# Performance work log

Measured on AMD Instinct MI355X. Metric: run time of the kernel, lower is better.

The kernel has to match this reference:

```python
import jax, jax.numpy as jnp
from jax import lax
import numpy as np
import math

B_SZ, SEQ, D_MODEL = 2, 2048, 2048
D_INNER, D_STATE, D_CONV, HEADS, P, CHUNK = 4096, 128, 4, 64, 64, 128
CONV_DIM = D_INNER + 2 * D_STATE
D_IN_PROJ = 2 * D_INNER + 2 * D_STATE + HEADS


def setup_inputs() -> dict:
    key = jax.random.key(0)
    ks = jax.random.split(key, 6)
    hidden_states = jax.random.normal(ks[0], (B_SZ, SEQ, D_MODEL), jnp.float32)
    W_in = jax.random.normal(ks[1], (D_IN_PROJ, D_MODEL), jnp.float32) * 0.02
    W_conv = jax.random.normal(ks[2], (CONV_DIM, 1, D_CONV), jnp.float32) * 0.2
    b_conv = jnp.zeros((CONV_DIM,), jnp.float32)
    A_log = jnp.log(jnp.arange(1, HEADS + 1, dtype=jnp.float32))
    D = jnp.ones((HEADS,), jnp.float32)
    # dt_bias init as in the torch module
    dt = jnp.exp(jax.random.uniform(ks[3], (HEADS,)) * (math.log(0.1) - math.log(0.001)) + math.log(0.001))
    dt = jnp.clip(dt, 1e-4, None)
    dt_bias = dt + jnp.log(-jnp.expm1(-dt))
    norm_weight = jnp.ones((D_INNER,), jnp.float32)
    W_out = jax.random.normal(ks[4], (D_MODEL, D_INNER), jnp.float32) * 0.02
    return {"hidden_states": hidden_states, "W_in": W_in, "W_conv": W_conv, "b_conv": b_conv,
            "A_log": A_log, "D": D, "dt_bias": dt_bias, "norm_weight": norm_weight, "W_out": W_out}


def _mamba2_core(hidden_states, W_in, W_conv, b_conv, A_log, D, dt_bias, norm_weight, W_out):
    Bsz, L, _ = hidden_states.shape
    NC = L // CHUNK
    zxbcdt = hidden_states @ W_in.T                         # [B,L,d_in_proj]
    z = zxbcdt[..., :D_INNER]
    xBC = zxbcdt[..., D_INNER:D_INNER + CONV_DIM]
    dt = zxbcdt[..., -HEADS:]
    # causal depthwise conv1d over sequence
    xc = jnp.swapaxes(xBC, 1, 2)                            # [B,C,L]
    xc = lax.conv_general_dilated(xc, W_conv, (1,), [(D_CONV - 1, 0)],
                                  feature_group_count=CONV_DIM,
                                  dimension_numbers=('NCH', 'OIH', 'NCH'))
    xc = xc + b_conv[None, :, None]
    xBC = jax.nn.silu(jnp.swapaxes(xc, 1, 2))               # [B,L,conv_dim]
    x = xBC[..., :D_INNER]
    Bm = xBC[..., D_INNER:D_INNER + D_STATE]                # num_groups=1
    Cm = xBC[..., -D_STATE:]
    dt = jax.nn.softplus(dt + dt_bias)                      # [B,L,H]; dt_limit (0,inf) is a no-op
    A = -jnp.exp(A_log)                                     # [H]
    # --- chunked SSD scan (chunk_size = CHUNK), same math as torch_ssm ---
    xch = x.reshape(Bsz, NC, CHUNK, HEADS, P)
    dtc = dt.reshape(Bsz, NC, CHUNK, HEADS)
    Bc = Bm.reshape(Bsz, NC, CHUNK, D_STATE)
    Cc = Cm.reshape(Bsz, NC, CHUNK, D_STATE)
    u = xch * dtc[..., None]                                # [b,c,l,h,p]
    dA = dtc * A                                            # [b,c,l,h]
    dA_cs = jnp.cumsum(dA, axis=2)                          # [b,c,l,h]
    # within-chunk causal attention-like term
    seg = dA_cs[:, :, :, None, :] - dA_cs[:, :, None, :, :] # [b,c,l,s,h]
    mask = jnp.tril(jnp.ones((CHUNK, CHUNK), bool))
    Lmat = jnp.exp(jnp.where(mask[None, None, :, :, None], seg, -jnp.inf))
    CB = jnp.einsum('bcln,bcsn->bcls', Cc, Bc)
    M = CB[..., None] * Lmat                                # [b,c,l,s,h]
    Y_diag = jnp.einsum('bclsh,bcshp->bclhp', M, u)
    # per-chunk final states
    decay_states = jnp.exp(dA_cs[:, :, -1:, :] - dA_cs)     # [b,c,l,h]
    states = jnp.einsum('bcln,bclh,bclhp->bchpn', Bc, decay_states, u)
    chunk_decay = jnp.exp(dA_cs[:, :, -1, :])               # [b,c,h]
    # inter-chunk recurrence over NC chunks
    def step(h, inp):
        st, cd = inp                                        # [b,h,p,n], [b,h]
        h_new = h * cd[:, :, None, None] + st
        return h_new, h                                     # emit state at chunk start
    sts = jnp.moveaxis(states, 1, 0)
    cds = jnp.moveaxis(chunk_decay, 1, 0)
    h0 = jnp.zeros((Bsz, HEADS, P, D_STATE), hidden_states.dtype)
    _, h_starts = lax.scan(step, h0, (sts, cds))
    h_starts = jnp.moveaxis(h_starts, 0, 1)                 # [b,c,h,p,n]
    state_decay_out = jnp.exp(dA_cs)                        # [b,c,l,h]
    Y_off = jnp.einsum('bcln,bclh,bchpn->bclhp', Cc, state_decay_out, h_starts)
    Y = Y_diag + Y_off + D[None, None, None, :, None] * xch
    y = Y.reshape(Bsz, L, D_INNER)
    # gated RMSNorm (gate first, then norm; group_size == d_inner)
    yg = y * jax.nn.silu(z)
    var = jnp.mean(yg * yg, axis=-1, keepdims=True)
    y = yg * lax.rsqrt(var + 1e-5) * norm_weight
    return y @ W_out.T


def reference(hidden_states, W_in, W_conv, b_conv, A_log, D, dt_bias, norm_weight, W_out):
    return _mamba2_core(hidden_states, W_in, W_conv, b_conv, A_log, D, dt_bias, norm_weight, W_out)
```

## Files before the change

kernel.cpp:

```cpp
#include <hip/hip_runtime.h>
#include <hip/hip_bf16.h>
#include <stdint.h>

typedef __bf16 bf16;
typedef __bf16 bf16x8 __attribute__((ext_vector_type(8)));
typedef __bf16 bf16x4 __attribute__((ext_vector_type(4)));
typedef float f32x4v __attribute__((ext_vector_type(4)));

#define SEQ    2048
#define DMODEL 2048
#define DI     4096
#define NH     64
#define PDIM   64
#define CHUNKL 128
#define NCH    16
#define CONVD  4352
#define DPROJ  8512
#define ZLD    8704
#define NTOK   4096
#define LP     136

__device__ __forceinline__ float sigmoid_f(float x){ return 1.f/(1.f+expf(-x)); }
__device__ __forceinline__ float silu_f(float x){ return x*sigmoid_f(x); }
__device__ __forceinline__ float softplus_f(float x){ return x > 20.f ? x : log1pf(expf(x)); }

__global__ __launch_bounds__(256) void cvt_all_kernel(const float* __restrict__ hs,
                                                      const float* __restrict__ W_in,
                                                      const float* __restrict__ W_out,
                                                      bf16* __restrict__ hsb,
                                                      bf16* __restrict__ winb,
                                                      bf16* __restrict__ woutb){
    int blk = blockIdx.x;
    if (blk < 8192){
        int i = (blk*256 + threadIdx.x)*4;
        float4 v = *(const float4*)&hs[i];
        bf16x4 o; o[0]=(bf16)v.x; o[1]=(bf16)v.y; o[2]=(bf16)v.z; o[3]=(bf16)v.w;
        *(bf16x4*)&hsb[i] = o;
    } else if (blk < 25600){
        int i = ((blk-8192)*256 + threadIdx.x)*4;
        int r = i >> 11;
        bf16x4 o;
        if (r < DPROJ){
            float4 v = *(const float4*)&W_in[i];
            o[0]=(bf16)v.x; o[1]=(bf16)v.y; o[2]=(bf16)v.z; o[3]=(bf16)v.w;
        } else {
            o[0]=(bf16)0.f; o[1]=(bf16)0.f; o[2]=(bf16)0.f; o[3]=(bf16)0.f;
        }
        *(bf16x4*)&winb[i] = o;
    } else {
        int i = ((blk-25600)*256 + threadIdx.x)*4;
        float4 v = *(const float4*)&W_out[i];
        bf16x4 o; o[0]=(bf16)v.x; o[1]=(bf16)v.y; o[2]=(bf16)v.z; o[3]=(bf16)v.w;
        *(bf16x4*)&woutb[i] = o;
    }
}

#define READ_A(BUFP, QM)                                                               \
    {                                                                                  \
        _Pragma("unroll")                                                              \
        for (int i=0;i<4;i++)                                                          \
            _Pragma("unroll")                                                          \
            for (int k2=0;k2<2;k2++)                                                   \
                af[i][k2] = *(const bf16x8*)&(BUFP)[aoff[i][k2] + (QM)*8192];          \
    }

#define READ_B(BUFP, QN, BFR)                                                          \
    {                                                                                  \
        _Pragma("unroll")                                                              \
        for (int nf=0;nf<2;nf++)                                                       \
            _Pragma("unroll")                                                          \
            for (int k2=0;k2<2;k2++)                                                   \
                BFR[nf][k2] = *(const bf16x8*)&(BUFP)[boff[nf][k2] + (QN)*8192];       \
    }

#define MMA_Q(QM, QN, BFR)                                                             \
    {                                                                                  \
        __builtin_amdgcn_s_setprio(1);                                                 \
        _Pragma("unroll")                                                              \
        for (int i=0;i<4;i++)                                                          \
            _Pragma("unroll")                                                          \
            for (int nf=0;nf<2;nf++)                                                   \
                _Pragma("unroll")                                                      \
                for (int k2=0;k2<2;k2++)                                               \
                    acc[(QM)*4+i][(QN)*2+nf] = __builtin_amdgcn_mfma_f32_16x16x32_bf16( \
                        af[i][k2], BFR[nf][k2], acc[(QM)*4+i][(QN)*2+nf], 0,0,0);      \
        __builtin_amdgcn_s_setprio(0);                                                 \
    }

#define SBAR() do { __builtin_amdgcn_sched_barrier(0);                                 \
                    __builtin_amdgcn_s_barrier();                                      \
                    asm volatile("s_waitcnt lgkmcnt(0)" ::: "memory");                 \
                    __builtin_amdgcn_sched_barrier(0); } while(0)

__global__ __launch_bounds__(512) void gemm1_kernel(const bf16* __restrict__ A,
                                                    const bf16* __restrict__ Bmat,
                                                    bf16* __restrict__ Cz,
                                                    float* __restrict__ tpart,
                                                    int NXB, int NYB, int K){
    __shared__ __align__(16) bf16 lds[2][2*16384];
    const int tid  = threadIdx.x;
    const int w    = tid >> 6;
    const int lane = tid & 63;
    const int wm   = w >> 2, wn = w & 3;
    const int bid  = blockIdx.x;

    int aoff[4][2], boff[2][2];
    #pragma unroll
    for (int i=0;i<4;i++)
        #pragma unroll
        for (int k2=0;k2<2;k2++){
            int ra0 = wm*64 + i*16 + (lane&15);
            int slot = (k2*4 + (lane>>4)) ^ (ra0&7);
            aoff[i][k2] = ra0*64 + slot*8;
        }
    #pragma unroll
    for (int nf=0;nf<2;nf++)
        #pragma unroll
        for (int k2=0;k2<2;k2++){
            int rb0 = wn*32 + nf*16 + (lane&15);
            int slot = (k2*4 + (lane>>4)) ^ (rb0&7);
            boff[nf][k2] = 16384 + rb0*64 + slot*8;
        }
    const int er = (lane>>4)*4, ec = lane&15;

    if (bid < 256){
        int kz  = bid >> 6;
        int t64 = bid & 63;
        const int tn2 = 8192 + (t64 & 3)*128;
        const int tm2 = (t64 >> 2)*256;
        const int kt0 = kz*8;

        const bf16* srcA2[2][2];
        const bf16* srcB2[2];
        #pragma unroll
        for (int r0h=0;r0h<2;r0h++)
            #pragma unroll
            for (int i=0;i<2;i++){
                int lr = r0h*128 + i*64 + (tid>>3);
                int growA = tm2 + ((lr>>6)&1)*128 + (lr>>7)*64 + (lr&63);
                int gslot = (tid&7) ^ (lr&7);
                srcA2[r0h][i] = A + (long)growA*K + gslot*8;
            }
        #pragma unroll
        for (int i=0;i<2;i++){
            int lr = i*64 + (tid>>3);
            int gslot = (tid&7) ^ (lr&7);
            srcB2[i] = Bmat + (long)(tn2 + lr)*K + gslot*8;
        }
        auto stA = [&](int buf, int t, int r0h){
            long koff = (long)(kt0 + t)*64;
            #pragma unroll
            for (int i=0;i<2;i++){
                bf16* dst = &lds[buf][0] + (size_t)(r0h*128 + i*64 + w*8)*64;
                __builtin_amdgcn_global_load_lds(
                    (const __attribute__((address_space(1))) void*)(srcA2[r0h][i] + koff),
                    (__attribute__((address_space(3))) void*)dst, 16, 0, 0);
            }
        };
        auto stB = [&](int buf, int t){
            long koff = (long)(kt0 + t)*64;
            #pragma unroll
            for (int i=0;i<2;i++){
                bf16* dst = &lds[buf][16384] + (size_t)(i*64 + w*8)*64;
                __builtin_amdgcn_global_load_lds(
                    (const __attribute__((address_space(1))) void*)(srcB2[i] + koff),
                    (__attribute__((address_space(3))) void*)dst, 16, 0, 0);
            }
        };

        f32x4v acc2[8][2];
        #pragma unroll
        for (int i=0;i<8;i++)
            #pragma unroll
            for (int j=0;j<2;j++) acc2[i][j] = {0.f,0.f,0.f,0.f};
        bf16x8 af[4][2], bfr0[2][2];

        stA(0,0,0); stA(0,0,1); stB(0,0);
        __syncthreads();
        int cur = 0;
        for (int t=0; t<8; ++t){
            int nxt = cur ^ 1;
            const bf16* bufc = &lds[cur][0];
            if (t+1 < 8){ stA(nxt,t+1,0); stA(nxt,t+1,1); stB(nxt,t+1); }
            READ_A(bufc, 0)
            READ_B(bufc, 0, bfr0)
            #pragma unroll
            for (int i=0;i<4;i++)
                #pragma unroll
                for (int nf=0;nf<2;nf++)
                    #pragma unroll
                    for (int k2=0;k2<2;k2++)
                        acc2[i][nf] = __builtin_amdgcn_mfma_f32_16x16x32_bf16(
                            af[i][k2], bfr0[nf][k2], acc2[i][nf], 0,0,0);
            READ_A(bufc, 1)
            #pragma unroll
            for (int i=0;i<4;i++)
                #pragma unroll
                for (int nf=0;nf<2;nf++)
                    #pragma unroll
                    for (int k2=0;k2<2;k2++)
                        acc2[4+i][nf] = __builtin_amdgcn_mfma_f32_16x16x32_bf16(
                            af[i][k2], bfr0[nf][k2], acc2[4+i][nf], 0,0,0);
            __syncthreads();
            cur = nxt;
        }
        #pragma unroll
        for (int mi=0;mi<8;mi++)
            #pragma unroll
            for (int nf=0;nf<2;nf++){
                long r0 = tm2 + wm*128 + mi*16 + er;
                int  c0 = tn2 + wn*32 + nf*16 + ec;
                #pragma unroll
                for (int j=0;j<4;j++)
                    tpart[((long)kz*4096 + (r0+j))*512 + (c0 - 8192)] = acc2[mi][nf][j];
            }
        return;
    }

    int bid2 = bid - 256;
    int wg   = (bid2 & 7)*64 + (bid2 >> 3);
    const int SW = 8;
    int sup = wg / (SW*NYB);
    int rr  = wg % (SW*NYB);
    int x0  = sup*SW;
    int wl  = (NXB - x0 < SW) ? (NXB - x0) : SW;
    int x   = x0 + rr % wl;
    int y   = rr / wl;
    const int tm = y*256, tn = x*256;
    const int KT = K >> 6;

    f32x4v acc[8][4];
    #pragma unroll
    for (int i=0;i<8;i++)
        #pragma unroll
        for (int j=0;j<4;j++) acc[i][j] = {0.f,0.f,0.f,0.f};
    bf16x8 af[4][2];
    bf16x8 bfr0[2][2], bfr1[2][2];

    const bf16* srcA[2][2];
    const bf16* srcB[2][2];
    #pragma unroll
    for (int r0h=0;r0h<2;r0h++)
        #pragma unroll
        for (int i=0;i<2;i++){
            int lr = r0h*128 + i*64 + (tid>>3);
            int growA = tm + ((lr>>6)&1)*128 + (lr>>7)*64 + (lr&63);
            int growB = tn + ((lr>>5)&3)*64 + (lr>>7)*32 + (lr&31);
            int gslot = (tid&7) ^ (lr&7);
            srcA[r0h][i] = A + (long)growA*K + gslot*8;
            srcB[r0h][i] = Bmat + (long)growB*K + gslot*8;
        }

    auto stageA = [&](int buf, int t, int r0h){
        long koff = (long)t*64;
        #pragma unroll
        for (int i=0;i<2;i++){
            bf16* dst = &lds[buf][0] + (size_t)(r0h*128 + i*64 + w*8)*64;
            __builtin_amdgcn_global_load_lds(
                (const __attribute__((address_space(1))) void*)(srcA[r0h][i] + koff),
                (__attribute__((address_space(3))) void*)dst, 16, 0, 0);
        }
    };
    auto stageB = [&](int buf, int t, int r0h){
        long koff = (long)t*64;
        #pragma unroll
        for (int i=0;i<2;i++){
            bf16* dst = &lds[buf][16384] + (size_t)(r0h*128 + i*64 + w*8)*64;
            __builtin_amdgcn_global_load_lds(
                (const __attribute__((address_space(1))) void*)(srcB[r0h][i] + koff),
                (__attribute__((address_space(3))) void*)dst, 16, 0, 0);
        }
    };

    stageA(0, 0, 0); stageB(0, 0, 0); stageA(0, 0, 1); stageB(0, 0, 1);
    if (KT > 1){ stageA(1, 1, 0); stageB(1, 1, 0); stageA(1, 1, 1); stageB(1, 1, 1); }
    asm volatile("s_waitcnt vmcnt(8)" ::: "memory");
    __builtin_amdgcn_s_barrier();

    int cur = 0;
    for (int t = 0; t < KT; ++t){
        int nxt = cur ^ 1;
        const bf16* bufc = &lds[cur][0];
        READ_A(bufc, 0)
        READ_B(bufc, 0, bfr0)
        READ_B(bufc, 1, bfr1)
        if (t+1 < KT){ asm volatile("s_waitcnt vmcnt(8)" ::: "memory"); }
        else         { asm volatile("s_waitcnt vmcnt(0)" ::: "memory"); }
        SBAR();
        MMA_Q(0, 0, bfr0)
        MMA_Q(0, 1, bfr1)
        __builtin_amdgcn_sched_barrier(0);
        if (t+2 < KT){ stageA(cur, t+2, 0); stageB(cur, t+2, 0); }
        READ_A(bufc, 1)
        SBAR();
        MMA_Q(1, 0, bfr0)
        MMA_Q(1, 1, bfr1)
        __builtin_amdgcn_sched_barrier(0);
        if (t+2 < KT){ stageA(cur, t+2, 1); stageB(cur, t+2, 1); }
        cur = nxt;
    }

    #pragma unroll
    for (int mi=0;mi<8;mi++)
        #pragma unroll
        for (int ni=0;ni<4;ni++){
            long r0 = tm + wm*128 + mi*16 + er;
            int  c0 = tn + wn*64 + ni*16 + ec;
            #pragma unroll
            for (int j=0;j<4;j++)
                Cz[(r0+j)*ZLD + c0] = (bf16)acc[mi][ni][j];
        }
}

__global__ __launch_bounds__(512) void gemm256x128_kernel(const bf16* __restrict__ A,
                                                          const bf16* __restrict__ Bmat,
                                                          float* __restrict__ C,
                                                          int NXB, int NYB, int K, int ldc){
    __shared__ __align__(16) bf16 lds[3][24576];
    const int tid  = threadIdx.x;
    const int w    = tid >> 6;
    const int lane = tid & 63;
    const int wm   = w >> 2, wn = w & 3;

    int bid = blockIdx.x, nb = gridDim.x;
    int wg = (bid & 7)*(nb >> 3) + (bid >> 3);
    const int SW = 8;
    int sup = wg / (SW*NYB);
    int rr  = wg % (SW*NYB);
    int x0  = sup*SW;
    int wl  = (NXB - x0 < SW) ? (NXB - x0) : SW;
    int x   = x0 + rr % wl;
    int y   = rr / wl;
    const int tm = y*256, tn = x*128;
    const int KT = K >> 6;

    f32x4v acc[8][2];
    #pragma unroll
    for (int i=0;i<8;i++)
        #pragma unroll
        for (int j=0;j<2;j++) acc[i][j] = {0.f,0.f,0.f,0.f};
    bf16x8 af[4][2];
    bf16x8 bfr[2][2];

    const bf16* srcA[2][2];
    const bf16* srcB[2];
    #pragma unroll
    for (int r0h=0;r0h<2;r0h++)
        #pragma unroll
        for (int i=0;i<2;i++){
            int lr = r0h*128 + i*64 + (tid>>3);
            int growA = tm + ((lr>>6)&1)*128 + (lr>>7)*64 + (lr&63);
            int gslot = (tid&7) ^ (lr&7);
            srcA[r0h][i] = A + (long)growA*K + gslot*8;
        }
    #pragma unroll
    for (int i=0;i<2;i++){
        int lr = i*64 + (tid>>3);
        int gslot = (tid&7) ^ (lr&7);
        srcB[i] = Bmat + (long)(tn + lr)*K + gslot*8;
    }
    int aoff[4][2], boff[2][2];
    #pragma unroll
    for (int i=0;i<4;i++)
        #pragma unroll
        for (int k2=0;k2<2;k2++){
            int ra0 = wm*64 + i*16 + (lane&15);
            int slot = (k2*4 + (lane>>4)) ^ (ra0&7);
            aoff[i][k2] = ra0*64 + slot*8;
        }
    #pragma unroll
    for (int nf=0;nf<2;nf++)
        #pragma unroll
        for (int k2=0;k2<2;k2++){
            int rb0 = wn*32 + nf*16 + (lane&15);
            int slot = (k2*4 + (lane>>4)) ^ (rb0&7);
            boff[nf][k2] = 16384 + rb0*64 + slot*8;
        }

    auto stageA = [&](int buf, int t, int r0h){
        long koff = (long)t*64;
        #pragma unroll
        for (int i=0;i<2;i++){
            bf16* dst = &lds[buf][0] + (size_t)(r0h*128 + i*64 + w*8)*64;
            __builtin_amdgcn_global_load_lds(
                (const __attribute__((address_space(1))) void*)(srcA[r0h][i] + koff),
                (__attribute__((address_space(3))) void*)dst, 16, 0, 0);
        }
    };
    auto stageB = [&](int buf, int t){
        long koff = (long)t*64;
        #pragma unroll
        for (int i=0;i<2;i++){
            bf16* dst = &lds[buf][16384] + (size_t)(i*64 + w*8)*64;
            __builtin_amdgcn_global_load_lds(
                (const __attribute__((address_space(1))) void*)(srcB[i] + koff),
                (__attribute__((address_space(3))) void*)dst, 16, 0, 0);
        }
    };

    stageA(0, 0, 0); stageA(0, 0, 1); stageB(0, 0);
    if (KT > 1){ stageA(1, 1, 0); stageA(1, 1, 1); stageB(1, 1); }
    asm volatile("s_waitcnt vmcnt(6)" ::: "memory");
    __builtin_amdgcn_s_barrier();

    int cur = 0;
    for (int t = 0; t < KT; ++t){
        int stb = cur + 2; if (stb >= 3) stb -= 3;
        const bf16* bufc = &lds[cur][0];
        READ_A(bufc, 0)
        READ_B(bufc, 0, bfr)
        if (t+2 < KT){ stageA(stb, t+2, 0); stageA(stb, t+2, 1); }
        SBAR();
        MMA_Q(0, 0, bfr)
        READ_A(bufc, 1)
        if (t+2 < KT){
            stageB(stb, t+2);
            asm volatile("s_waitcnt vmcnt(6)" ::: "memory");
        } else {
            asm volatile("s_waitcnt vmcnt(0)" ::: "memory");
        }
        SBAR();
        MMA_Q(1, 0, bfr)
        cur = (cur == 2) ? 0 : cur + 1;
    }

    const int er = (lane>>4)*4, ec = lane&15;
    #pragma unroll
    for (int mi=0;mi<8;mi++)
        #pragma unroll
        for (int ni=0;ni<2;ni++){
            long r0 = tm + wm*128 + mi*16 + er;
            int  c0 = tn + wn*32 + ni*16 + ec;
            #pragma unroll
            for (int j=0;j<4;j++)
                C[(r0+j)*ldc + c0] = acc[mi][ni][j];
        }
}

__global__ __launch_bounds__(256) void tailreduce_kernel(const float* __restrict__ p,
                                                         bf16* __restrict__ zx,
                                                         float* __restrict__ dtf){
    long i = ((long)blockIdx.x*256 + threadIdx.x)*4;
    int r = (int)(i >> 9);
    int c = (int)(i & 511);
    const long Q = (long)4096*512;
    float4 a  = *(const float4*)&p[i];
    float4 b  = *(const float4*)&p[i+Q];
    float4 cc = *(const float4*)&p[i+2*Q];
    float4 d  = *(const float4*)&p[i+3*Q];
    float s0 = a.x+b.x+cc.x+d.x, s1 = a.y+b.y+cc.y+d.y;
    float s2 = a.z+b.z+cc.z+d.z, s3 = a.w+b.w+cc.w+d.w;
    bf16x4 o; o[0]=(bf16)s0; o[1]=(bf16)s1; o[2]=(bf16)s2; o[3]=(bf16)s3;
    *(bf16x4*)&zx[(long)r*ZLD + 8192 + c] = o;
    int col = 8192 + c;
    float sv[4] = {s0,s1,s2,s3};
    #pragma unroll
    for (int j=0;j<4;j++){
        int cj = col + j;
        if (cj >= 8448 && cj < 8512) dtf[(long)r*64 + (cj-8448)] = sv[j];
    }
}

__global__ __launch_bounds__(256) void mid1_kernel(const bf16* __restrict__ zx,
                                                   const float* __restrict__ Wc,
                                                   const float* __restrict__ bc,
                                                   const float* __restrict__ dtf,
                                                   const float* __restrict__ A_log,
                                                   const float* __restrict__ dt_bias,
                                                   bf16* __restrict__ xc,
                                                   float* __restrict__ dtv,
                                                   float* __restrict__ dacs,
                                                   float* __restrict__ cdec){
    int blk = blockIdx.x;
    if (blk < 2560){
        int by = blk/5, bx = blk%5;
        int c4 = bx*256 + threadIdx.x;
        if (c4 >= 1088) return;
        int ch = c4*4;
        int b = by >> 8, t0 = (by & 255)*8;
        float4 tap[4];
        #pragma unroll
        for (int e=0;e<4;e++) tap[e] = *(const float4*)&Wc[(ch+e)*4];
        float4 bq = *(const float4*)&bc[ch];
        float bca[4] = {bq.x, bq.y, bq.z, bq.w};
        const bf16* col = zx + (long)(b*SEQ)*ZLD + 4096 + ch;
        bf16x4 v[11];
        #pragma unroll
        for (int k=0;k<11;k++){
            int t = t0 - 3 + k;
            if (t >= 0) v[k] = *(const bf16x4*)&col[(long)t*ZLD];
            else { v[k][0]=(bf16)0.f; v[k][1]=(bf16)0.f; v[k][2]=(bf16)0.f; v[k][3]=(bf16)0.f; }
        }
        #pragma unroll
        for (int j=0;j<8;j++){
            bf16x4 o;
            #pragma unroll
            for (int e=0;e<4;e++){
                float acc = bca[e] + (float)v[j][e]*tap[e].x + (float)v[j+1][e]*tap[e].y
                                   + (float)v[j+2][e]*tap[e].z + (float)v[j+3][e]*tap[e].w;
                o[e] = (bf16)silu_f(acc);
            }
            *(bf16x4*)&xc[(long)(b*SEQ + t0 + j)*CONVD + ch] = o;
        }
    } else {
        int wid  = ((blk-2560)*256 + threadIdx.x) >> 6;
        int lane = threadIdx.x & 63;
        int h  = wid & 63, bc2 = wid >> 6;
        int b  = bc2 >> 4,  c  = bc2 & 15;
        float Ah   = -expf(A_log[h]);
        float bias = dt_bias[h];
        long tok0 = (long)(b*SEQ + c*CHUNKL);
        int l0 = lane*2;
        float d0 = softplus_f(dtf[(tok0+l0)*64 + h] + bias);
        float d1 = softplus_f(dtf[(tok0+l0+1)*64 + h] + bias);
        float s = (d0 + d1)*Ah;
        #pragma unroll
        for (int off=1; off<64; off<<=1){
            float t = __shfl_up(s, off, 64);
            if (lane >= off) s += t;
        }
        long base_h = (long)wid*128;
        float cs1 = s;
        float cs0 = s - d1*Ah;
        dtv[base_h+l0]   = d0;  dtv[base_h+l0+1]  = d1;
        dacs[base_h+l0]  = cs0; dacs[base_h+l0+1] = cs1;
        if (lane == 63) cdec[wid] = expf(cs1);
    }
}

__global__ __launch_bounds__(256) void cb_mfma_kernel(const bf16* __restrict__ xc,
                                                      float* __restrict__ cb,
                                                      bf16* __restrict__ BT){
    __shared__ __align__(16) bf16 A1[128*LP];
    __shared__ __align__(16) bf16 B1[128*LP];
    int blk = blockIdx.x;  int b = blk>>4, c = blk&15;
    int tid = threadIdx.x;
    const int w = tid >> 6, lane = tid & 63;
    long tok0 = (long)(b*SEQ + c*CHUNKL);
    int l = tid>>1, n0 = (tid&1)*64;
    const bf16* crow = xc + tok0*CONVD + (long)l*CONVD;
    #pragma unroll
    for (int v=0;v<8;v++){
        *(bf16x8*)&A1[l*LP + n0 + v*8] = *(const bf16x8*)&crow[4224 + n0 + v*8];
        *(bf16x8*)&B1[l*LP + n0 + v*8] = *(const bf16x8*)&crow[4096 + n0 + v*8];
    }
    __syncthreads();
    f32x4v acc[2][8];
    #pragma unroll
    for (int mi=0;mi<2;mi++)
        #pragma unroll
        for (int ni=0;ni<8;ni++) acc[mi][ni] = {0.f,0.f,0.f,0.f};
    #pragma unroll
    for (int kk=0; kk<128; kk+=32){
        bf16x8 afr[2], bfr2[8];
        #pragma unroll
        for (int mi=0;mi<2;mi++)
            afr[mi] = *(const bf16x8*)&A1[(w*32 + mi*16 + (lane&15))*LP + kk + (lane>>4)*8];
        #pragma unroll
        for (int ni=0;ni<8;ni++)
            bfr2[ni] = *(const bf16x8*)&B1[(ni*16 + (lane&15))*LP + kk + (lane>>4)*8];
        #pragma unroll
        for (int mi=0;mi<2;mi++)
            #pragma unroll
            for (int ni=0;ni<8;ni++)
                acc[mi][ni] = __builtin_amdgcn_mfma_f32_16x16x32_bf16(afr[mi], bfr2[ni], acc[mi][ni], 0,0,0);
    }
    float* out = cb + (long)blk*16384;
    #pragma unroll
    for (int mi=0;mi<2;mi++)
        #pragma unroll
        for (int ni=0;ni<8;ni++){
            int r0 = w*32 + mi*16 + (lane>>4)*4;
            int c0 = ni*16 + (lane&15);
            #pragma unroll
            for (int j=0;j<4;j++) out[(long)(r0+j)*128 + c0] = acc[mi][ni][j];
        }
    {
        int n = tid>>1, s0 = (tid&1)*64;
        bf16* btp = BT + (long)blk*16384 + (long)n*128 + s0;
        #pragma unroll
        for (int v=0;v<8;v++){
            bf16x8 o;
            #pragma unroll
            for (int e=0;e<8;e++) o[e] = B1[(s0+v*8+e)*LP + n];
            *(bf16x8*)&btp[v*8] = o;
        }
    }
}

__global__ __launch_bounds__(256) void states_mfma_kernel(const bf16* __restrict__ xc,
                                                          const bf16* __restrict__ BT,
                                                          const float* __restrict__ dtv,
                                                          const float* __restrict__ dacs,
                                                          bf16* __restrict__ states){
    __shared__ __align__(16) bf16 A1[64*LP];
    __shared__ __align__(16) bf16 B1[128*LP];
    __shared__ float wgtl[128];
    int blk = blockIdx.x;
    int h = blk & 63, bc = blk >> 6;
    int b = bc >> 4, c = bc & 15;
    int tid = threadIdx.x;
    const int w = tid >> 6, lane = tid & 63;
    long tok0 = (long)(b*SEQ + c*CHUNKL);
    long base_h = (long)blk*128;
    float cs_last = dacs[base_h + 127];
    if (tid < 128) wgtl[tid] = dtv[base_h+tid] * expf(cs_last - dacs[base_h+tid]);
    __syncthreads();
    #pragma unroll
    for (int t=0;t<4;t++){
        int l = (tid>>3) + t*32;
        int p0 = (tid&7)*8;
        bf16x8 xv = *(const bf16x8*)&xc[(tok0+l)*CONVD + h*64 + p0];
        float wv = wgtl[l];
        #pragma unroll
        for (int e=0;e<8;e++) A1[(p0+e)*LP + l] = (bf16)((float)xv[e]*wv);
    }
    {
        int n = tid>>1, l0 = (tid&1)*64;
        const bf16* btp = BT + (long)bc*16384 + (long)n*128 + l0;
        #pragma unroll
        for (int v=0;v<8;v++)
            *(bf16x8*)&B1[n*LP + l0 + v*8] = *(const bf16x8*)&btp[v*8];
    }
    __syncthreads();
    f32x4v acc[8];
    #pragma unroll
    for (int ni=0;ni<8;ni++) acc[ni] = {0.f,0.f,0.f,0.f};
    #pragma unroll
    for (int kk=0; kk<128; kk+=32){
        bf16x8 afr = *(const bf16x8*)&A1[(w*16 + (lane&15))*LP + kk + (lane>>4)*8];
        #pragma unroll
        for (int ni=0;ni<8;ni++){
            bf16x8 bfr2 = *(const bf16x8*)&B1[(ni*16 + (lane&15))*LP + kk + (lane>>4)*8];
            acc[ni] = __builtin_amdgcn_mfma_f32_16x16x32_bf16(afr, bfr2, acc[ni], 0,0,0);
        }
    }
    bf16* out = states + (long)blk*8192;
    #pragma unroll
    for (int ni=0;ni<8;ni++){
        int p0 = w*16 + (lane>>4)*4;
        int n  = ni*16 + (lane&15);
        #pragma unroll
        for (int j=0;j<4;j++) out[(long)(p0+j)*128 + n] = (bf16)acc[ni][j];
    }
}

__global__ __launch_bounds__(256) void scan_kernel(const bf16* __restrict__ states,
                                                   const float* __restrict__ cdec,
                                                   bf16* __restrict__ hst){
    long gid = (long)blockIdx.x*256 + threadIdx.x;
    int n = gid & 127;
    int p = (gid >> 7) & 63;
    int h = (gid >> 13) & 63;
    int b = (int)(gid >> 19);
    float hrun = 0.f;
    for (int c=0;c<16;c++){
        long idx = ((((long)(b*16 + c)*64 + h)*64 + p)*128) + n;
        hst[idx] = (bf16)hrun;
        hrun = hrun * cdec[(b*16+c)*64 + h] + (float)states[idx];
    }
}

__global__ __launch_bounds__(256) void yfused_kernel(const bf16* __restrict__ xc,
                                                     const float* __restrict__ cb,
                                                     const bf16* __restrict__ hst,
                                                     const float* __restrict__ dtv,
                                                     const float* __restrict__ dacs,
                                                     bf16* __restrict__ Ybf){
    __shared__ __align__(16) bf16 A1[128*LP];
    __shared__ __align__(16) bf16 B1[64*LP];
    __shared__ float csl[128];
    int blk = blockIdx.x;
    int h = blk & 63, bc = blk >> 6;
    int b = bc >> 4, c = bc & 15;
    int tid = threadIdx.x;
    const int w = tid >> 6, lane = tid & 63;
    long tok0 = (long)(b*SEQ + c*CHUNKL);
    long base_h = (long)blk*128;
    if (tid < 128) csl[tid] = dacs[base_h + tid];
    __syncthreads();
    {
        int l = tid>>1, s0 = (tid&1)*64;
        float el = csl[l];
        const float* cbrow = cb + (long)bc*16384 + (long)l*128 + s0;
        int jend = l - s0; if (jend > 63) jend = 63;
        for (int j=0; j<=jend; j++)
            A1[l*LP + s0 + j] = (bf16)(cbrow[j]*expf(el - csl[s0+j]));
        for (int j=jend+1; j<64; j++)
            A1[l*LP + s0 + j] = (bf16)0.f;
    }
    #pragma unroll
    for (int t=0;t<4;t++){
        int s = (tid>>3) + t*32;
        int p0 = (tid&7)*8;
        bf16x8 xv = *(const bf16x8*)&xc[(tok0+s)*CONVD + h*64 + p0];
        float wv = dtv[base_h + s];
        #pragma unroll
        for (int e=0;e<8;e++) B1[(p0+e)*LP + s] = (bf16)((float)xv[e]*wv);
    }
    __syncthreads();
    f32x4v acc[2][4];
    #pragma unroll
    for (int mi=0;mi<2;mi++)
        #pragma unroll
        for (int ni=0;ni<4;ni++) acc[mi][ni] = {0.f,0.f,0.f,0.f};
    #pragma unroll
    for (int kk=0; kk<128; kk+=32){
        bf16x8 afr[2], bfr2[4];
        #pragma unroll
        for (int mi=0;mi<2;mi++)
            afr[mi] = *(const bf16x8*)&A1[(w*32 + mi*16 + (lane&15))*LP + kk + (lane>>4)*8];
        #pragma unroll
        for (int ni=0;ni<4;ni++)
            bfr2[ni] = *(const bf16x8*)&B1[(ni*16 + (lane&15))*LP + kk + (lane>>4)*8];
        #pragma unroll
        for (int mi=0;mi<2;mi++)
            #pragma unroll
            for (int ni=0;ni<4;ni++)
                acc[mi][ni] = __builtin_amdgcn_mfma_f32_16x16x32_bf16(afr[mi], bfr2[ni], acc[mi][ni], 0,0,0);
    }
    __syncthreads();
    {
        int l = tid>>1, n0 = (tid&1)*64;
        float e1 = expf(csl[l]);
        const bf16* crow = xc + (tok0+l)*CONVD + 4224;
        #pragma unroll
        for (int v=0;v<8;v++){
            bf16x8 cv = *(const bf16x8*)&crow[n0 + v*8];
            bf16x8 o;
            #pragma unroll
            for (int e=0;e<8;e++) o[e] = (bf16)((float)cv[e]*e1);
            *(bf16x8*)&A1[l*LP + n0 + v*8] = o;
        }
    }
    {
        int p = tid>>2, n0 = (tid&3)*32;
        const bf16* hrow = hst + (long)blk*8192 + (long)p*128 + n0;
        #pragma unroll
        for (int v=0;v<4;v++)
            *(bf16x8*)&B1[p*LP + n0 + v*8] = *(const bf16x8*)&hrow[v*8];
    }
    __syncthreads();
    #pragma unroll
    for (int kk=0; kk<128; kk+=32){
        bf16x8 afr[2], bfr2[4];
        #pragma unroll
        for (int mi=0;mi<2;mi++)
            afr[mi] = *(const bf16x8*)&A1[(w*32 + mi*16 + (lane&15))*LP + kk + (lane>>4)*8];
        #pragma unroll
        for (int ni=0;ni<4;ni++)
            bfr2[ni] = *(const bf16x8*)&B1[(ni*16 + (lane&15))*LP + kk + (lane>>4)*8];
        #pragma unroll
        for (int mi=0;mi<2;mi++)
            #pragma unroll
            for (int ni=0;ni<4;ni++)
                acc[mi][ni] = __builtin_amdgcn_mfma_f32_16x16x32_bf16(afr[mi], bfr2[ni], acc[mi][ni], 0,0,0);
    }
    #pragma unroll
    for (int mi=0;mi<2;mi++)
        #pragma unroll
        for (int ni=0;ni<4;ni++){
            int l0 = w*32 + mi*16 + (lane>>4)*4;
            int p  = ni*16 + (lane&15);
            #pragma unroll
            for (int j=0;j<4;j++)
                Ybf[(tok0 + l0 + j)*DI + h*64 + p] = (bf16)acc[mi][ni][j];
        }
}

__global__ __launch_bounds__(256) void gatenorm_kernel(const bf16* __restrict__ Ybf,
                                                       const bf16* __restrict__ zx,
                                                       const bf16* __restrict__ xc,
                                                       const float* __restrict__ Dp,
                                                       const float* __restrict__ nw,
                                                       bf16* __restrict__ ybn){
    __shared__ float red[4];
    int tok = blockIdx.x, tid = threadIdx.x;
    const bf16* yrow = Ybf + (long)tok*DI;
    const bf16* zrow = zx  + (long)tok*ZLD;
    const bf16* xrow = xc  + (long)tok*CONVD;
    float yg[16];
    float ss = 0.f;
    #pragma unroll
    for (int k=0;k<2;k++){
        int d = (tid + k*256)*8;
        bf16x8 yv = *(const bf16x8*)&yrow[d];
        bf16x8 zv = *(const bf16x8*)&zrow[d];
        bf16x8 xv = *(const bf16x8*)&xrow[d];
        float dh = Dp[d>>6];
        #pragma unroll
        for (int e=0;e<8;e++){
            float yy = (float)yv[e] + dh*(float)xv[e];
            float g = yy*silu_f((float)zv[e]);
            yg[k*8+e] = g;
            ss += g*g;
        }
    }
    #pragma unroll
    for (int off=32; off>0; off>>=1) ss += __shfl_down(ss, off, 64);
    if ((tid & 63) == 0) red[tid>>6] = ss;
    __syncthreads();
    float tot = red[0]+red[1]+red[2]+red[3];
    float scale = rsqrtf(tot/(float)DI + 1e-5f);
    #pragma unroll
    for (int k=0;k<2;k++){
        int d = (tid + k*256)*8;
        float4 w0 = *(const float4*)&nw[d];
        float4 w1 = *(const float4*)&nw[d+4];
        float wv[8] = {w0.x,w0.y,w0.z,w0.w,w1.x,w1.y,w1.z,w1.w};
        bf16x8 o;
        #pragma unroll
        for (int e=0;e<8;e++) o[e] = (bf16)(yg[k*8+e]*scale*wv[e]);
        *(bf16x8*)&ybn[(long)tok*DI + d] = o;
    }
}

extern "C" void kernel_launch(void* const* d_in, const int* in_sizes, int n_in,
                              void* d_out, int out_size, void* d_ws, size_t ws_size,
                              hipStream_t stream){
    const float* hs      = (const float*)d_in[0];
    const float* W_in    = (const float*)d_in[1];
    const float* W_conv  = (const float*)d_in[2];
    const float* b_conv  = (const float*)d_in[3];
    const float* A_log   = (const float*)d_in[4];
    const float* Dp      = (const float*)d_in[5];
    const float* dt_bias = (const float*)d_in[6];
    const float* nw      = (const float*)d_in[7];
    const float* W_out   = (const float*)d_in[8];
    float* out = (float*)d_out;

    char* ws = (char*)d_ws;
    const size_t OFF_ZX    = 0;
    const size_t OFF_DTF   = 71303168;
    const size_t OFF_XC    = 72351744;
    const size_t OFF_DTV   = 108003328;
    const size_t OFF_DACS  = 109051904;
    const size_t OFF_CDEC  = 110100480;
    const size_t OFF_CB    = 110108672;
    const size_t OFF_SLOTA = 112205824;
    const size_t OFF_SLOTB = 179314688;
    const size_t OFF_WOUTB = 212869120;

    bf16*  zx    = (bf16*)(ws + OFF_ZX);
    float* dtf   = (float*)(ws + OFF_DTF);
    bf16*  xc    = (bf16*)(ws + OFF_XC);
    float* dtv   = (float*)(ws + OFF_DTV);
    float* dacs  = (float*)(ws + OFF_DACS);
    float* cdec  = (float*)(ws + OFF_CDEC);
    float* cbuf  = (float*)(ws + OFF_CB);
    bf16*  hsb   = (bf16*)(ws + OFF_SLOTA);
    bf16*  winb  = (bf16*)(ws + OFF_SLOTA + 16777216);
    bf16*  states= (bf16*)(ws + OFF_SLOTA);
    bf16*  Ybf   = (bf16*)(ws + OFF_SLOTA);
    float* tpart = (float*)(ws + OFF_SLOTB);
    bf16*  BTb   = (bf16*)(ws + OFF_SLOTB);
    bf16*  hst   = (bf16*)(ws + OFF_SLOTB);
    bf16*  ybn   = (bf16*)(ws + OFF_SLOTB);
    bf16*  woutb = (bf16*)(ws + OFF_WOUTB);

    cvt_all_kernel<<<33792, 256, 0, stream>>>(hs, W_in, W_out, hsb, winb, woutb);

    gemm1_kernel<<<768, 512, 0, stream>>>(hsb, winb, zx, tpart, 32, 16, DMODEL);
    tailreduce_kernel<<<2048, 256, 0, stream>>>(tpart, zx, dtf);

    mid1_kernel<<<3072, 256, 0, stream>>>(zx, W_conv, b_conv, dtf, A_log, dt_bias,
                                          xc, dtv, dacs, cdec);
    cb_mfma_kernel<<<32, 256, 0, stream>>>(xc, cbuf, BTb);
    states_mfma_kernel<<<2048, 256, 0, stream>>>(xc, BTb, dtv, dacs, states);
    scan_kernel<<<4096, 256, 0, stream>>>(states, cdec, hst);
    yfused_kernel<<<2048, 256, 0, stream>>>(xc, cbuf, hst, dtv, dacs, Ybf);
    gatenorm_kernel<<<4096, 256, 0, stream>>>(Ybf, zx, xc, Dp, nw, ybn);

    gemm256x128_kernel<<<256, 512, 0, stream>>>(ybn, woutb, out, 16, 16, DI, DMODEL);
}
```

Baseline: 373.2 us.

## Fuse chunk states, scan and output into one kernel; re-pipeline GEMM loads

Three kernels (per-chunk state MFMA, inter-chunk scan, and the intra/inter-chunk output) are replaced by one kernel. Each block owns a (batch, head, half-P) slice, walks the 16 chunks in order and keeps the running state in registers, so the states and hst intermediates no longer round-trip through global memory and two launches disappear. The trade is only 256 blocks of 512 threads with a serial chunk loop, which lowers parallelism and may underfill the GPU. Separately, the gemm1 main loop is re-pipelined: the wait-count and barrier sit at the top of each iteration, stage loads are reordered and issued earlier, and LDS waits are explicit.

```diff
diff --git a/kernel.cpp b/kernel.cpp
--- a/kernel.cpp
+++ b/kernel.cpp
@@ -272,31 +272,36 @@
         }
     };
 
-    stageA(0, 0, 0); stageB(0, 0, 0); stageA(0, 0, 1); stageB(0, 0, 1);
-    if (KT > 1){ stageA(1, 1, 0); stageB(1, 1, 0); stageA(1, 1, 1); stageB(1, 1, 1); }
-    asm volatile("s_waitcnt vmcnt(8)" ::: "memory");
-    __builtin_amdgcn_s_barrier();
+    stageA(0, 0, 0); stageB(0, 0, 0); stageB(0, 0, 1); stageA(0, 0, 1);
+    if (KT > 1){ stageA(1, 1, 0); stageB(1, 1, 0); stageB(1, 1, 1); }
 
     int cur = 0;
     for (int t = 0; t < KT; ++t){
         int nxt = cur ^ 1;
         const bf16* bufc = &lds[cur][0];
+        if (t+1 < KT){ asm volatile("s_waitcnt vmcnt(6)" ::: "memory"); }
+        else         { asm volatile("s_waitcnt vmcnt(0)" ::: "memory"); }
+        __builtin_amdgcn_sched_barrier(0);
+        __builtin_amdgcn_s_barrier();
+        __builtin_amdgcn_sched_barrier(0);
+        if (t+1 < KT) stageA(nxt, t+1, 1);
         READ_A(bufc, 0)
         READ_B(bufc, 0, bfr0)
         READ_B(bufc, 1, bfr1)
-        if (t+1 < KT){ asm volatile("s_waitcnt vmcnt(8)" ::: "memory"); }
-        else         { asm volatile("s_waitcnt vmcnt(0)" ::: "memory"); }
-        SBAR();
+        asm volatile("s_waitcnt lgkmcnt(0)" ::: "memory");
+        __builtin_amdgcn_sched_barrier(0);
         MMA_Q(0, 0, bfr0)
         MMA_Q(0, 1, bfr1)
         __builtin_amdgcn_sched_barrier(0);
-        if (t+2 < KT){ stageA(cur, t+2, 0); stageB(cur, t+2, 0); }
+        __builtin_amdgcn_s_barrier();
+        __builtin_amdgcn_sched_barrier(0);
+        if (t+2 < KT){ stageA(cur, t+2, 0); stageB(cur, t+2, 0); stageB(cur, t+2, 1); }
         READ_A(bufc, 1)
-        SBAR();
+        asm volatile("s_waitcnt lgkmcnt(0)" ::: "memory");
+        __builtin_amdgcn_sched_barrier(0);
         MMA_Q(1, 0, bfr0)
         MMA_Q(1, 1, bfr1)
         __builtin_amdgcn_sched_barrier(0);
-        if (t+2 < KT){ stageA(cur, t+2, 1); stageB(cur, t+2, 1); }
         cur = nxt;
     }
 
@@ -588,184 +593,131 @@
     }
 }
 
-__global__ __launch_bounds__(256) void states_mfma_kernel(const bf16* __restrict__ xc,
-                                                          const bf16* __restrict__ BT,
-                                                          const float* __restrict__ dtv,
-                                                          const float* __restrict__ dacs,
-                                                          bf16* __restrict__ states){
-    __shared__ __align__(16) bf16 A1[64*LP];
-    __shared__ __align__(16) bf16 B1[128*LP];
-    __shared__ float wgtl[128];
+#define LPF 136
+__global__ __launch_bounds__(512) void chunkfused_kernel(const bf16* __restrict__ xc,
+                                                         const float* __restrict__ cbuf,
+                                                         const bf16* __restrict__ BT,
+                                                         const float* __restrict__ dtv,
+                                                         const float* __restrict__ dacs,
+                                                         bf16* __restrict__ Ybf){
+    __shared__ __align__(16) bf16 S_C[128*LPF];
+    __shared__ __align__(16) bf16 S_B[128*LPF];
+    __shared__ __align__(16) bf16 S_xu[32*LPF];
+    __shared__ __align__(16) bf16 S_xw[32*LPF];
+    __shared__ __align__(16) bf16 S_h[32*LPF];
+    __shared__ float csl[128];
+    __shared__ float dts[128];
     int blk = blockIdx.x;
-    int h = blk & 63, bc = blk >> 6;
-    int b = bc >> 4, c = bc & 15;
+    int ph = blk & 1, h = (blk>>1) & 63, b = blk >> 7;
     int tid = threadIdx.x;
     const int w = tid >> 6, lane = tid & 63;
-    long tok0 = (long)(b*SEQ + c*CHUNKL);
-    long base_h = (long)blk*128;
-    float cs_last = dacs[base_h + 127];
-    if (tid < 128) wgtl[tid] = dtv[base_h+tid] * expf(cs_last - dacs[base_h+tid]);
-    __syncthreads();
-    #pragma unroll
-    for (int t=0;t<4;t++){
-        int l = (tid>>3) + t*32;
-        int p0 = (tid&7)*8;
-        bf16x8 xv = *(const bf16x8*)&xc[(tok0+l)*CONVD + h*64 + p0];
-        float wv = wgtl[l];
-        #pragma unroll
-        for (int e=0;e<8;e++) A1[(p0+e)*LP + l] = (bf16)((float)xv[e]*wv);
-    }
-    {
-        int n = tid>>1, l0 = (tid&1)*64;
-        const bf16* btp = BT + (long)bc*16384 + (long)n*128 + l0;
-        #pragma unroll
-        for (int v=0;v<8;v++)
-            *(bf16x8*)&B1[n*LP + l0 + v*8] = *(const bf16x8*)&btp[v*8];
-    }
-    __syncthreads();
-    f32x4v acc[8];
-    #pragma unroll
-    for (int ni=0;ni<8;ni++) acc[ni] = {0.f,0.f,0.f,0.f};
-    #pragma unroll
-    for (int kk=0; kk<128; kk+=32){
-        bf16x8 afr = *(const bf16x8*)&A1[(w*16 + (lane&15))*LP + kk + (lane>>4)*8];
-        #pragma unroll
-        for (int ni=0;ni<8;ni++){
-            bf16x8 bfr2 = *(const bf16x8*)&B1[(ni*16 + (lane&15))*LP + kk + (lane>>4)*8];
-            acc[ni] = __builtin_amdgcn_mfma_f32_16x16x32_bf16(afr, bfr2, acc[ni], 0,0,0);
-        }
-    }
-    bf16* out = states + (long)blk*8192;
-    #pragma unroll
-    for (int ni=0;ni<8;ni++){
-        int p0 = w*16 + (lane>>4)*4;
-        int n  = ni*16 + (lane&15);
-        #pragma unroll
-        for (int j=0;j<4;j++) out[(long)(p0+j)*128 + n] = (bf16)acc[ni][j];
-    }
-}
-
-__global__ __launch_bounds__(256) void scan_kernel(const bf16* __restrict__ states,
-                                                   const float* __restrict__ cdec,
-                                                   bf16* __restrict__ hst){
-    long gid = (long)blockIdx.x*256 + threadIdx.x;
-    int n = gid & 127;
-    int p = (gid >> 7) & 63;
-    int h = (gid >> 13) & 63;
-    int b = (int)(gid >> 19);
-    float hrun = 0.f;
-    for (int c=0;c<16;c++){
-        long idx = ((((long)(b*16 + c)*64 + h)*64 + p)*128) + n;
-        hst[idx] = (bf16)hrun;
-        hrun = hrun * cdec[(b*16+c)*64 + h] + (float)states[idx];
-    }
-}
-
-__global__ __launch_bounds__(256) void yfused_kernel(const bf16* __restrict__ xc,
-                                                     const float* __restrict__ cb,
-                                                     const bf16* __restrict__ hst,
-                                                     const float* __restrict__ dtv,
-                                                     const float* __restrict__ dacs,
-                                                     bf16* __restrict__ Ybf){
-    __shared__ __align__(16) bf16 A1[128*LP];
-    __shared__ __align__(16) bf16 B1[64*LP];
-    __shared__ float csl[128];
-    int blk = blockIdx.x;
-    int h = blk & 63, bc = blk >> 6;
-    int b = bc >> 4, c = bc & 15;
-    int tid = threadIdx.x;
-    const int w = tid >> 6, lane = tid & 63;
-    long tok0 = (long)(b*SEQ + c*CHUNKL);
-    long base_h = (long)blk*128;
-    if (tid < 128) csl[tid] = dacs[base_h + tid];
-    __syncthreads();
-    {
-        int l = tid>>1, s0 = (tid&1)*64;
-        float el = csl[l];
-        const float* cbrow = cb + (long)bc*16384 + (long)l*128 + s0;
-        int jend = l - s0; if (jend > 63) jend = 63;
-        for (int j=0; j<=jend; j++)
-            A1[l*LP + s0 + j] = (bf16)(cbrow[j]*expf(el - csl[s0+j]));
-        for (int j=jend+1; j<64; j++)
-            A1[l*LP + s0 + j] = (bf16)0.f;
-    }
-    #pragma unroll
-    for (int t=0;t<4;t++){
-        int s = (tid>>3) + t*32;
-        int p0 = (tid&7)*8;
-        bf16x8 xv = *(const bf16x8*)&xc[(tok0+s)*CONVD + h*64 + p0];
-        float wv = dtv[base_h + s];
-        #pragma unroll
-        for (int e=0;e<8;e++) B1[(p0+e)*LP + s] = (bf16)((float)xv[e]*wv);
-    }
-    __syncthreads();
-    f32x4v acc[2][4];
-    #pragma unroll
-    for (int mi=0;mi<2;mi++)
-        #pragma unroll
-        for (int ni=0;ni<4;ni++) acc[mi][ni] = {0.f,0.f,0.f,0.f};
-    #pragma unroll
-    for (int kk=0; kk<128; kk+=32){
-        bf16x8 afr[2], bfr2[4];
-        #pragma unroll
-        for (int mi=0;mi<2;mi++)
-            afr[mi] = *(const bf16x8*)&A1[(w*32 + mi*16 + (lane&15))*LP + kk + (lane>>4)*8];
-        #pragma unroll
-        for (int ni=0;ni<4;ni++)
-            bfr2[ni] = *(const bf16x8*)&B1[(ni*16 + (lane&15))*LP + kk + (lane>>4)*8];
-        #pragma unroll
-        for (int mi=0;mi<2;mi++)
-            #pragma unroll
-            for (int ni=0;ni<4;ni++)
-                acc[mi][ni] = __builtin_amdgcn_mfma_f32_16x16x32_bf16(afr[mi], bfr2[ni], acc[mi][ni], 0,0,0);
-    }
-    __syncthreads();
-    {
-        int l = tid>>1, n0 = (tid&1)*64;
-        float e1 = expf(csl[l]);
-        const bf16* crow = xc + (tok0+l)*CONVD + 4224;
-        #pragma unroll
-        for (int v=0;v<8;v++){
-            bf16x8 cv = *(const bf16x8*)&crow[n0 + v*8];
-            bf16x8 o;
-            #pragma unroll
-            for (int e=0;e<8;e++) o[e] = (bf16)((float)cv[e]*e1);
-            *(bf16x8*)&A1[l*LP + n0 + v*8] = o;
-        }
-    }
-    {
-        int p = tid>>2, n0 = (tid&3)*32;
-        const bf16* hrow = hst + (long)blk*8192 + (long)p*128 + n0;
-        #pragma unroll
-        for (int v=0;v<4;v++)
-            *(bf16x8*)&B1[p*LP + n0 + v*8] = *(const bf16x8*)&hrow[v*8];
-    }
-    __syncthreads();
-    #pragma unroll
-    for (int kk=0; kk<128; kk+=32){
-        bf16x8 afr[2], bfr2[4];
-        #pragma unroll
-        for (int mi=0;mi<2;mi++)
-            afr[mi] = *(const bf16x8*)&A1[(w*32 + mi*16 + (lane&15))*LP + kk + (lane>>4)*8];
-        #pragma unroll
-        for (int ni=0;ni<4;ni++)
-            bfr2[ni] = *(const bf16x8*)&B1[(ni*16 + (lane&15))*LP + kk + (lane>>4)*8];
-        #pragma unroll
-        for (int mi=0;mi<2;mi++)
-            #pragma unroll
-            for (int ni=0;ni<4;ni++)
-                acc[mi][ni] = __builtin_amdgcn_mfma_f32_16x16x32_bf16(afr[mi], bfr2[ni], acc[mi][ni], 0,0,0);
-    }
-    #pragma unroll
-    for (int mi=0;mi<2;mi++)
-        #pragma unroll
-        for (int ni=0;ni<4;ni++){
-            int l0 = w*32 + mi*16 + (lane>>4)*4;
-            int p  = ni*16 + (lane&15);
+    const int pt = w >> 2, nb0 = (w & 3)*32;
+    const int Lb = w*16;
+    const int P0 = ph*32;
+
+    f32x4v h_run[2];
+    h_run[0] = {0.f,0.f,0.f,0.f}; h_run[1] = {0.f,0.f,0.f,0.f};
+
+    for (int c = 0; c < 16; ++c){
+        int bc = b*16 + c;
+        long tok0 = (long)(b*SEQ + c*CHUNKL);
+        long base_h = ((long)bc*64 + h)*128;
+        if (tid < 128) csl[tid] = dacs[base_h + tid];
+        else if (tid < 256) dts[tid-128] = dtv[base_h + tid - 128];
+        __syncthreads();
+        #pragma unroll
+        for (int t=0;t<2;t++)
             #pragma unroll
             for (int j=0;j<4;j++)
-                Ybf[(tok0 + l0 + j)*DI + h*64 + p] = (bf16)acc[mi][ni][j];
-        }
+                S_h[(pt*16 + (lane>>4)*4 + j)*LPF + nb0 + t*16 + (lane&15)] = (bf16)h_run[t][j];
+        {
+            int l = tid>>2, nq = tid&3;
+            float e1 = expf(csl[l]);
+            const bf16* crow = xc + (tok0+l)*CONVD + 4224 + nq*32;
+            #pragma unroll
+            for (int v2=0; v2<4; v2++){
+                bf16x8 cv = *(const bf16x8*)&crow[v2*8];
+                bf16x8 o;
+                #pragma unroll
+                for (int e=0;e<8;e++) o[e] = (bf16)((float)cv[e]*e1);
+                *(bf16x8*)&S_C[l*LPF + nq*32 + v2*8] = o;
+            }
+            const bf16* btp = BT + (long)bc*16384 + (long)l*128 + nq*32;
+            #pragma unroll
+            for (int v2=0; v2<4; v2++)
+                *(bf16x8*)&S_B[l*LPF + nq*32 + v2*8] = *(const bf16x8*)&btp[v2*8];
+        }
+        __syncthreads();
+        f32x4v acc_y[2];
+        acc_y[0] = {0.f,0.f,0.f,0.f}; acc_y[1] = {0.f,0.f,0.f,0.f};
+        #pragma unroll
+        for (int kk=0; kk<128; kk+=32){
+            bf16x8 afr = *(const bf16x8*)&S_C[(Lb + (lane&15))*LPF + kk + (lane>>4)*8];
+            #pragma unroll
+            for (int pt2=0; pt2<2; pt2++){
+                bf16x8 bfr = *(const bf16x8*)&S_h[(pt2*16 + (lane&15))*LPF + kk + (lane>>4)*8];
+                acc_y[pt2] = __builtin_amdgcn_mfma_f32_16x16x32_bf16(afr, bfr, acc_y[pt2], 0,0,0);
+            }
+        }
+        __syncthreads();
+        {
+            int l = tid>>2, s0 = (tid&3)*32;
+            float el = csl[l];
+            const float* cbrow = cbuf + (long)bc*16384 + (long)l*128 + s0;
+            #pragma unroll 8
+            for (int j=0;j<32;j++){
+                int s = s0 + j;
+                float v = (s <= l) ? cbrow[j]*expf(el - csl[s]) : 0.f;
+                S_C[l*LPF + s] = (bf16)v;
+            }
+            int s = tid & 127, pq = tid>>7;
+            bf16x8 xv = *(const bf16x8*)&xc[(tok0+s)*CONVD + h*64 + P0 + pq*8];
+            float us = dts[s];
+            float ws_ = us * expf(csl[127] - csl[s]);
+            #pragma unroll
+            for (int e=0;e<8;e++){
+                float xf = (float)xv[e];
+                S_xu[(pq*8+e)*LPF + s] = (bf16)(xf*us);
+                S_xw[(pq*8+e)*LPF + s] = (bf16)(xf*ws_);
+            }
+        }
+        __syncthreads();
+        f32x4v st[2];
+        st[0] = {0.f,0.f,0.f,0.f}; st[1] = {0.f,0.f,0.f,0.f};
+        #pragma unroll
+        for (int kk=0; kk<128; kk+=32){
+            bf16x8 afr = *(const bf16x8*)&S_C[(Lb + (lane&15))*LPF + kk + (lane>>4)*8];
+            #pragma unroll
+            for (int pt2=0; pt2<2; pt2++){
+                bf16x8 bfr = *(const bf16x8*)&S_xu[(pt2*16 + (lane&15))*LPF + kk + (lane>>4)*8];
+                acc_y[pt2] = __builtin_amdgcn_mfma_f32_16x16x32_bf16(afr, bfr, acc_y[pt2], 0,0,0);
+            }
+            bf16x8 af2 = *(const bf16x8*)&S_xw[(pt*16 + (lane&15))*LPF + kk + (lane>>4)*8];
+            #pragma unroll
+            for (int t=0;t<2;t++){
+                bf16x8 bf2 = *(const bf16x8*)&S_B[((nb0 + t*16) + (lane&15))*LPF + kk + (lane>>4)*8];
+                st[t] = __builtin_amdgcn_mfma_f32_16x16x32_bf16(af2, bf2, st[t], 0,0,0);
+            }
+        }
+        {
+            float cdc = expf(csl[127]);
+            #pragma unroll
+            for (int pt2=0; pt2<2; pt2++){
+                int pg = h*64 + P0 + pt2*16 + (lane&15);
+                #pragma unroll
+                for (int j=0;j<4;j++){
+                    long l = Lb + (lane>>4)*4 + j;
+                    Ybf[(tok0 + l)*DI + pg] = (bf16)acc_y[pt2][j];
+                }
+            }
+            #pragma unroll
+            for (int t=0;t<2;t++)
+                #pragma unroll
+                for (int j=0;j<4;j++)
+                    h_run[t][j] = h_run[t][j]*cdc + st[t][j];
+        }
+        __syncthreads();
+    }
 }
 
 __global__ __launch_bounds__(256) void gatenorm_kernel(const bf16* __restrict__ Ybf,
@@ -850,11 +802,9 @@
     float* cbuf  = (float*)(ws + OFF_CB);
     bf16*  hsb   = (bf16*)(ws + OFF_SLOTA);
     bf16*  winb  = (bf16*)(ws + OFF_SLOTA + 16777216);
-    bf16*  states= (bf16*)(ws + OFF_SLOTA);
     bf16*  Ybf   = (bf16*)(ws + OFF_SLOTA);
     float* tpart = (float*)(ws + OFF_SLOTB);
     bf16*  BTb   = (bf16*)(ws + OFF_SLOTB);
-    bf16*  hst   = (bf16*)(ws + OFF_SLOTB);
     bf16*  ybn   = (bf16*)(ws + OFF_SLOTB);
     bf16*  woutb = (bf16*)(ws + OFF_WOUTB);
 
@@ -866,9 +816,7 @@
     mid1_kernel<<<3072, 256, 0, stream>>>(zx, W_conv, b_conv, dtf, A_log, dt_bias,
                                           xc, dtv, dacs, cdec);
     cb_mfma_kernel<<<32, 256, 0, stream>>>(xc, cbuf, BTb);
-    states_mfma_kernel<<<2048, 256, 0, stream>>>(xc, BTb, dtv, dacs, states);
-    scan_kernel<<<4096, 256, 0, stream>>>(states, cdec, hst);
-    yfused_kernel<<<2048, 256, 0, stream>>>(xc, cbuf, hst, dtv, dacs, Ybf);
+    chunkfused_kernel<<<256, 512, 0, stream>>>(xc, cbuf, BTb, dtv, dacs, Ybf);
     gatenorm_kernel<<<4096, 256, 0, stream>>>(Ybf, zx, xc, Dp, nw, ybn);
 
     gemm256x128_kernel<<<256, 512, 0, stream>>>(ybn, woutb, out, 16, 16, DI, DMODEL);
```

Measured after the change: 471.5 us. +26.3%, slower.
